# Kernel optimization log

Hardware: AMD Instinct MI355X
Metric: run time of the kernel (lower is better)

## Reference

```python
import jax, jax.numpy as jnp
import numpy as np

NHEAD = 16
EPS = 1e-6

def _phi_norm(x):
    # phi = silu, then L2 normalize over last dim (torch F.normalize: x / max(||x||, eps))
    x = jax.nn.silu(x)
    n = jnp.linalg.norm(x, axis=-1, keepdims=True)
    return x / jnp.maximum(n, EPS)

def setup_inputs() -> dict:
    key = jax.random.key(0)
    k1, k2, k3 = jax.random.split(key, 3)
    B, M, N, D = 4, 1024, 2048, 1024
    q = jax.random.normal(k1, (B, M, D), dtype=jnp.float32)
    kv = jax.random.normal(k2, (B, N, D), dtype=jnp.float32)
    kv_mask = jax.random.bernoulli(k3, 0.1, (B, N))  # True = masked out
    return {"q": q, "kv": kv, "kv_mask": kv_mask}

def reference(q, kv, kv_mask):
    B, M, D = q.shape
    N = kv.shape[1]
    dh = D // NHEAD
    # [B, H, M, dh] / [B, H, N, dh]
    qh = q.reshape(B, M, NHEAD, dh).transpose(0, 2, 1, 3)
    kh = kv.reshape(B, N, NHEAD, dh).transpose(0, 2, 1, 3)
    vh = kh  # values are raw kv heads (no phi/norm)
    qh_n = _phi_norm(qh)
    kh_n = _phi_norm(kh)
    scores = jnp.einsum('bhmd,bhnd->bhmn', qh_n, kh_n) / jnp.sqrt(jnp.asarray(dh, qh_n.dtype))
    scores = jnp.where(kv_mask[:, None, None, :], -jnp.inf, scores)
    attn = jax.nn.softmax(scores.astype(jnp.float32), axis=-1).astype(scores.dtype)
    out = jnp.einsum('bhmn,bhnd->bhmd', attn, vh)
    return out.transpose(0, 2, 1, 3).reshape(B, M, D)
```

## Files before the change

kernel.cpp:

```cpp
#include <hip/hip_runtime.h>
#include <hip/hip_bf16.h>
#include <cmath>
#include <stdint.h>

#define B_ 4
#define M_ 1024
#define N_ 2048
#define D_ 1024
#define H_ 16
#define DH_ 64
#define NT 64
#define NTH 16
#define PITCH 72

typedef __bf16 bf16_t;
typedef __attribute__((ext_vector_type(8))) __bf16 bf16x8;
typedef __attribute__((ext_vector_type(16))) float f32x16;

static __device__ __forceinline__ float silu_f(float x) {
  return x / (1.0f + __expf(-x));
}

#if __has_builtin(__builtin_amdgcn_exp2f)
#define EXP2F(x) __builtin_amdgcn_exp2f(x)
#else
#define EXP2F(x) __expf((x) * 0.69314718056f)
#endif

static __device__ __forceinline__ unsigned pk2(float a, float b) {
  union { __bf16 h[2]; unsigned u; } p;
  p.h[0] = (__bf16)a; p.h[1] = (__bf16)b;
  return p.u;
}

static __device__ __forceinline__ void pl32swap(unsigned &x, unsigned &y) {
  asm("s_nop 0\n\tv_permlane32_swap_b32 %0, %1" : "+v"(x), "+v"(y));
}

static __device__ __forceinline__ void gload16(const bf16_t* g, bf16_t* l) {
  typedef __attribute__((address_space(1))) const unsigned GU;
  typedef __attribute__((address_space(3))) unsigned LU;
  __builtin_amdgcn_global_load_lds((GU*)(const unsigned*)g, (LU*)(unsigned*)l,
                                   16, 0, 0);
}

__global__ __launch_bounds__(256) void prep_kernel(
    const float* __restrict__ kv, const int* __restrict__ kv_mask,
    bf16_t* __restrict__ kp, bf16_t* __restrict__ vt,
    unsigned long long* __restrict__ mb) {
  __shared__ __align__(16) bf16_t Lt[NT][PITCH];
  const int bx = blockIdx.x;
  const int hp = bx & 7;
  const int nt = (bx >> 3) & 31;
  const int b  = bx >> 8;
  const int n0 = nt * NT;
  const int tid = threadIdx.x;
  const float keep = kv_mask[b * N_ + n0 + (tid >> 2)] ? 0.f : 1.f;

  #pragma unroll
  for (int hi = 0; hi < 2; ++hi) {
    const int h = hp * 2 + hi;
    const size_t bh = (size_t)(b * H_ + h);
    {
      const int r = tid >> 2, c0 = (tid & 3) * 16;
      const float* src = kv + ((size_t)(b * N_ + n0 + r)) * D_ + h * DH_ + c0;
      union { float f[16]; float4 v4[4]; } raw;
      raw.v4[0] = *(const float4*)(src + 0);
      raw.v4[1] = *(const float4*)(src + 4);
      raw.v4[2] = *(const float4*)(src + 8);
      raw.v4[3] = *(const float4*)(src + 12);
      float sv[16];
      float ss = 0.f;
      #pragma unroll
      for (int i = 0; i < 16; ++i) { sv[i] = silu_f(raw.f[i]); ss += sv[i] * sv[i]; }
      ss += __shfl_xor(ss, 1); ss += __shfl_xor(ss, 2);
      const float inv = keep / fmaxf(sqrtf(ss), 1e-6f);
      union { bf16_t bs[16]; uint4 u[2]; } pk;
      #pragma unroll
      for (int i = 0; i < 16; ++i) pk.bs[i] = (bf16_t)(sv[i] * inv);
      uint4* kdst = (uint4*)(kp + (bh * N_ + n0 + r) * DH_ + c0);
      kdst[0] = pk.u[0]; kdst[1] = pk.u[1];
      union { bf16_t bs[16]; uint4 u[2]; } pv;
      #pragma unroll
      for (int i = 0; i < 16; ++i) pv.bs[i] = (bf16_t)(raw.f[i] * keep);
      uint4* ldst = (uint4*)&Lt[r][c0];
      ldst[0] = pv.u[0]; ldst[1] = pv.u[1];
    }
    __syncthreads();
    {
      const int d = tid >> 2, nc = (tid & 3) * 16;
      union { bf16_t bs[16]; uint4 u[2]; } pk;
      #pragma unroll
      for (int i = 0; i < 16; ++i) pk.bs[i] = Lt[nc + i][d];
      uint4* dst = (uint4*)(vt + (bh * DH_ + d) * N_ + n0 + nc);
      dst[0] = pk.u[0]; dst[1] = pk.u[1];
    }
    __syncthreads();
  }
  if (bx == 0 && tid < B_ * (N_ / 64)) {
    const int b2 = tid >> 5, tt = tid & 31;
    unsigned long long m = 0ull;
    for (int i = 0; i < 64; ++i)
      if (kv_mask[b2 * N_ + tt * 64 + i]) m |= (1ull << i);
    mb[tid] = m;
  }
}

__global__ __launch_bounds__(512, 4) void attn_kernel(
    const float* __restrict__ q, const bf16_t* __restrict__ kp,
    const bf16_t* __restrict__ vt, const unsigned long long* __restrict__ mb,
    float* __restrict__ out) {
  __shared__ __align__(1024) char smem[65536];

  const int tid  = threadIdx.x;
  const int w    = tid >> 6;
  const int wq   = w & 3;
  const int half = w >> 2;
  const int lane = tid & 63;
  const int l31  = lane & 31;
  const int hi   = lane >> 5;
  const int rho  = l31 & 7;

  const int wg = (blockIdx.x & 7) * 64 + (blockIdx.x >> 3);
  const int bh = wg >> 3;
  const int m0 = (wg & 7) * 128;
  const int b = bh >> 4, h = bh & 15;

  const bf16_t* kpb = kp + (size_t)bh * N_ * DH_ + (size_t)half * NTH * NT * DH_;
  const bf16_t* vtb = vt + (size_t)bh * DH_ * N_;

  const int srow  = lane >> 3;
  const int sslot = (lane & 7) ^ srow;
  const bf16_t* ks0 = kpb + (size_t)(wq * 16 + srow) * DH_ + sslot * 8;
  const bf16_t* ks1 = ks0 + 8 * DH_;
  const bf16_t* vs0 = vtb + (size_t)(wq * 16 + srow) * N_ + half * NTH * NT + sslot * 8;
  const bf16_t* vs1 = vs0 + 8 * N_;

  {
    bf16_t* Kd = (bf16_t*)(smem + (half * 2 + 0) * 8192) + wq * 16 * DH_;
    bf16_t* Vd = (bf16_t*)(smem + 32768 + (half * 2 + 0) * 8192) + wq * 16 * NT;
    gload16(ks0, Kd); gload16(ks1, Kd + 512);
    gload16(vs0, Vd); gload16(vs1, Vd + 512);
  }

  bf16x8 qb[4];
  {
    const float* qrow =
        q + ((size_t)(b * M_ + m0 + wq * 32 + l31)) * D_ + h * DH_ + hi * 8;
    float sv[32];
    float ss = 0.f;
    #pragma unroll
    for (int kk = 0; kk < 4; ++kk) {
      float4 a0 = *(const float4*)(qrow + kk * 16);
      float4 a1 = *(const float4*)(qrow + kk * 16 + 4);
      sv[kk * 8 + 0] = silu_f(a0.x); sv[kk * 8 + 1] = silu_f(a0.y);
      sv[kk * 8 + 2] = silu_f(a0.z); sv[kk * 8 + 3] = silu_f(a0.w);
      sv[kk * 8 + 4] = silu_f(a1.x); sv[kk * 8 + 5] = silu_f(a1.y);
      sv[kk * 8 + 6] = silu_f(a1.z); sv[kk * 8 + 7] = silu_f(a1.w);
      #pragma unroll
      for (int i = 0; i < 8; ++i) ss += sv[kk * 8 + i] * sv[kk * 8 + i];
    }
    ss += __shfl_xor(ss, 32);
    const float inv = 1.0f / fmaxf(sqrtf(ss), 1e-6f);
    #pragma unroll
    for (int kk = 0; kk < 4; ++kk) {
      union { unsigned u[4]; bf16x8 v; } pq;
      #pragma unroll
      for (int jj = 0; jj < 4; ++jj)
        pq.u[jj] = pk2(sv[kk * 8 + jj * 2] * inv, sv[kk * 8 + jj * 2 + 1] * inv);
      qb[kk] = pq.v;
    }
  }

  int foff[2][4];
  #pragma unroll
  for (int i = 0; i < 2; ++i)
    #pragma unroll
    for (int j = 0; j < 4; ++j)
      foff[i][j] = (i * 32 + l31) * 64 + ((((j << 1) + hi) ^ rho) << 3);

  f32x16 o0, o1;
  #pragma unroll
  for (int r = 0; r < 16; ++r) { o0[r] = 0.f; o1[r] = 0.f; }
  float lrun = 0.f;
  unsigned cl = 0, ch = 0;
  const unsigned long long* mbb = mb + b * (N_ / 64);
  const float C1 = 0.125f * 1.44269504f;

  for (int tt = 0; tt < NTH; ++tt) {
    __syncthreads();
    const int cur = tt & 1;
    if (tt + 1 < NTH) {
      const int nx = cur ^ 1;
      const size_t ko = (size_t)(tt + 1) * NT * DH_;
      const size_t vo = (size_t)(tt + 1) * NT;
      bf16_t* Kd = (bf16_t*)(smem + (half * 2 + nx) * 8192) + wq * 16 * DH_;
      bf16_t* Vd = (bf16_t*)(smem + 32768 + (half * 2 + nx) * 8192) + wq * 16 * NT;
      gload16(ks0 + ko, Kd); gload16(ks1 + ko, Kd + 512);
      gload16(vs0 + vo, Vd); gload16(vs1 + vo, Vd + 512);
    }
    const unsigned long long mk = mbb[half * NTH + tt];
    cl += (unsigned)__popcll(mk & 0x0F0F0F0F0F0F0F0FULL);
    ch += (unsigned)__popcll(mk & 0xF0F0F0F0F0F0F0F0ULL);

    const bf16_t* Kc = (const bf16_t*)(smem + (half * 2 + cur) * 8192);
    const bf16_t* Vc = (const bf16_t*)(smem + 32768 + (half * 2 + cur) * 8192);

    bf16x8 pa[4];
    #pragma unroll
    for (int nb = 0; nb < 2; ++nb) {
      f32x16 s;
      #pragma unroll
      for (int r = 0; r < 16; ++r) s[r] = 0.f;
      __builtin_amdgcn_s_setprio(1);
      #pragma unroll
      for (int kk = 0; kk < 4; ++kk) {
        bf16x8 ka = *(const bf16x8*)(Kc + foff[nb][kk]);
        s = __builtin_amdgcn_mfma_f32_32x32x16_bf16(ka, qb[kk], s, 0, 0, 0);
      }
      __builtin_amdgcn_s_setprio(0);

      float p[16];
      #pragma unroll
      for (int r = 0; r < 16; ++r) p[r] = EXP2F(s[r] * C1);
      lrun += (((p[0] + p[1]) + (p[2] + p[3])) + ((p[4] + p[5]) + (p[6] + p[7]))) +
              (((p[8] + p[9]) + (p[10] + p[11])) + ((p[12] + p[13]) + (p[14] + p[15])));

      unsigned pkw[4][2];
      #pragma unroll
      for (int qq = 0; qq < 4; ++qq) {
        pkw[qq][0] = pk2(p[qq * 4 + 0], p[qq * 4 + 1]);
        pkw[qq][1] = pk2(p[qq * 4 + 2], p[qq * 4 + 3]);
      }
      #pragma unroll
      for (int tp = 0; tp < 2; ++tp) {
        union { unsigned u[4]; bf16x8 v; } fr;
        #pragma unroll
        for (int ww = 0; ww < 2; ++ww) {
          const unsigned own = hi ? pkw[2 * tp + 1][ww] : pkw[2 * tp][ww];
          unsigned x = hi ? pkw[2 * tp][ww] : pkw[2 * tp + 1][ww];
          unsigned y = x;
          pl32swap(x, y);
          fr.u[ww]     = hi ? x : own;
          fr.u[2 + ww] = hi ? own : y;
        }
        pa[nb * 2 + tp] = fr.v;
      }
    }

    __builtin_amdgcn_s_setprio(1);
    #pragma unroll
    for (int ks = 0; ks < 4; ++ks) {
      bf16x8 vb0 = *(const bf16x8*)(Vc + foff[0][ks]);
      bf16x8 vb1 = *(const bf16x8*)(Vc + foff[1][ks]);
      o0 = __builtin_amdgcn_mfma_f32_32x32x16_bf16(pa[ks], vb0, o0, 0, 0, 0);
      o1 = __builtin_amdgcn_mfma_f32_32x32x16_bf16(pa[ks], vb1, o1, 0, 0, 0);
    }
    __builtin_amdgcn_s_setprio(0);
  }

  lrun -= (float)(hi ? ch : cl);
  __syncthreads();
  lrun += __shfl_xor(lrun, 32);
  float* Ob = (float*)smem;
  float* Lb = (float*)(smem + 32768);

  if (half == 0) {
    #pragma unroll
    for (int r = 0; r < 16; ++r) {
      const int mrow = (r & 3) + ((r >> 2) << 3) + (hi << 2);
      Ob[(wq * 32 + mrow) * 64 + l31]      = o0[r];
      Ob[(wq * 32 + mrow) * 64 + 32 + l31] = o1[r];
    }
    if (hi == 0) Lb[wq * 32 + l31] = lrun;
  }
  __syncthreads();
  if (half == 1) {
    const float ltot = lrun + Lb[wq * 32 + l31];
    #pragma unroll
    for (int r = 0; r < 16; ++r) {
      const int mrow = (r & 3) + ((r >> 2) << 3) + (hi << 2);
      const float lv = __shfl(ltot, mrow);
      const float iv = lv > 0.f ? 1.0f / lv : 0.f;
      const float oa = Ob[(wq * 32 + mrow) * 64 + l31];
      const float oc = Ob[(wq * 32 + mrow) * 64 + 32 + l31];
      const size_t base =
          ((size_t)(b * M_ + m0 + wq * 32 + mrow)) * D_ + h * DH_ + l31;
      out[base]      = (o0[r] + oa) * iv;
      out[base + 32] = (o1[r] + oc) * iv;
    }
  }
}

extern "C" void kernel_launch(void* const* d_in, const int* in_sizes, int n_in,
                              void* d_out, int out_size, void* d_ws, size_t ws_size,
                              hipStream_t stream) {
  const float* q  = (const float*)d_in[0];
  const float* kv = (const float*)d_in[1];
  const int* kv_mask = (const int*)d_in[2];
  float* out = (float*)d_out;

  bf16_t* kp = (bf16_t*)d_ws;
  bf16_t* vt = kp + (size_t)B_ * H_ * N_ * DH_;
  unsigned long long* mb =
      (unsigned long long*)((char*)d_ws + 2 * (size_t)B_ * H_ * N_ * DH_ * sizeof(bf16_t));

  prep_kernel<<<B_ * 32 * 8, 256, 0, stream>>>(kv, kv_mask, kp, vt, mb);
  attn_kernel<<<B_ * H_ * (M_ / 128), 512, 0, stream>>>(q, kp, vt, mb, out);
}
```

Baseline: 147.3 us.

## Replace exp2 with quadratic polynomial, permute K rows to drop permlane swaps

New measurement: 146.9 us. About the same (-0.3%).

```diff
diff --git a/kernel.cpp b/kernel.cpp
--- a/kernel.cpp
+++ b/kernel.cpp
@@ -16,25 +16,16 @@
 typedef __bf16 bf16_t;
 typedef __attribute__((ext_vector_type(8))) __bf16 bf16x8;
 typedef __attribute__((ext_vector_type(16))) float f32x16;
+typedef __attribute__((ext_vector_type(2))) float f32x2;
 
 static __device__ __forceinline__ float silu_f(float x) {
   return x / (1.0f + __expf(-x));
 }
-
-#if __has_builtin(__builtin_amdgcn_exp2f)
-#define EXP2F(x) __builtin_amdgcn_exp2f(x)
-#else
-#define EXP2F(x) __expf((x) * 0.69314718056f)
-#endif
 
 static __device__ __forceinline__ unsigned pk2(float a, float b) {
   union { __bf16 h[2]; unsigned u; } p;
   p.h[0] = (__bf16)a; p.h[1] = (__bf16)b;
   return p.u;
-}
-
-static __device__ __forceinline__ void pl32swap(unsigned &x, unsigned &y) {
-  asm("s_nop 0\n\tv_permlane32_swap_b32 %0, %1" : "+v"(x), "+v"(y));
 }
 
 static __device__ __forceinline__ void gload16(const bf16_t* g, bf16_t* l) {
@@ -42,6 +33,10 @@
   typedef __attribute__((address_space(3))) unsigned LU;
   __builtin_amdgcn_global_load_lds((GU*)(const unsigned*)g, (LU*)(unsigned*)l,
                                    16, 0, 0);
+}
+
+static __device__ __forceinline__ int sw23(int x) {
+  return (x & ~12) | ((x & 4) << 1) | ((x & 8) >> 1);
 }
 
 __global__ __launch_bounds__(256) void prep_kernel(
@@ -131,8 +126,8 @@
 
   const int srow  = lane >> 3;
   const int sslot = (lane & 7) ^ srow;
-  const bf16_t* ks0 = kpb + (size_t)(wq * 16 + srow) * DH_ + sslot * 8;
-  const bf16_t* ks1 = ks0 + 8 * DH_;
+  const bf16_t* ks0 = kpb + (size_t)sw23(wq * 16 + srow) * DH_ + sslot * 8;
+  const bf16_t* ks1 = kpb + (size_t)sw23(wq * 16 + 8 + srow) * DH_ + sslot * 8;
   const bf16_t* vs0 = vtb + (size_t)(wq * 16 + srow) * N_ + half * NTH * NT + sslot * 8;
   const bf16_t* vs1 = vs0 + 8 * N_;
 
@@ -161,7 +156,7 @@
       for (int i = 0; i < 8; ++i) ss += sv[kk * 8 + i] * sv[kk * 8 + i];
     }
     ss += __shfl_xor(ss, 32);
-    const float inv = 1.0f / fmaxf(sqrtf(ss), 1e-6f);
+    const float inv = 0.125f / fmaxf(sqrtf(ss), 1e-6f);
     #pragma unroll
     for (int kk = 0; kk < 4; ++kk) {
       union { unsigned u[4]; bf16x8 v; } pq;
@@ -179,13 +174,12 @@
     for (int j = 0; j < 4; ++j)
       foff[i][j] = (i * 32 + l31) * 64 + ((((j << 1) + hi) ^ rho) << 3);
 
-  f32x16 o0, o1;
+  f32x16 o0, o1, zvec;
   #pragma unroll
-  for (int r = 0; r < 16; ++r) { o0[r] = 0.f; o1[r] = 0.f; }
+  for (int r = 0; r < 16; ++r) { o0[r] = 0.f; o1[r] = 0.f; zvec[r] = 0.f; }
   float lrun = 0.f;
   unsigned cl = 0, ch = 0;
   const unsigned long long* mbb = mb + b * (N_ / 64);
-  const float C1 = 0.125f * 1.44269504f;
 
   for (int tt = 0; tt < NTH; ++tt) {
     __syncthreads();
@@ -200,8 +194,8 @@
       gload16(vs0 + vo, Vd); gload16(vs1 + vo, Vd + 512);
     }
     const unsigned long long mk = mbb[half * NTH + tt];
-    cl += (unsigned)__popcll(mk & 0x0F0F0F0F0F0F0F0FULL);
-    ch += (unsigned)__popcll(mk & 0xF0F0F0F0F0F0F0F0ULL);
+    cl += (unsigned)__popcll(mk & 0x00FF00FF00FF00FFULL);
+    ch += (unsigned)__popcll(mk & 0xFF00FF00FF00FF00ULL);
 
     const bf16_t* Kc = (const bf16_t*)(smem + (half * 2 + cur) * 8192);
     const bf16_t* Vc = (const bf16_t*)(smem + 32768 + (half * 2 + cur) * 8192);
@@ -209,43 +203,36 @@
     bf16x8 pa[4];
     #pragma unroll
     for (int nb = 0; nb < 2; ++nb) {
-      f32x16 s;
-      #pragma unroll
-      for (int r = 0; r < 16; ++r) s[r] = 0.f;
       __builtin_amdgcn_s_setprio(1);
-      #pragma unroll
-      for (int kk = 0; kk < 4; ++kk) {
+      f32x16 s = __builtin_amdgcn_mfma_f32_32x32x16_bf16(
+          *(const bf16x8*)(Kc + foff[nb][0]), qb[0], zvec, 0, 0, 0);
+      #pragma unroll
+      for (int kk = 1; kk < 4; ++kk) {
         bf16x8 ka = *(const bf16x8*)(Kc + foff[nb][kk]);
         s = __builtin_amdgcn_mfma_f32_32x32x16_bf16(ka, qb[kk], s, 0, 0, 0);
       }
       __builtin_amdgcn_s_setprio(0);
 
-      float p[16];
-      #pragma unroll
-      for (int r = 0; r < 16; ++r) p[r] = EXP2F(s[r] * C1);
-      lrun += (((p[0] + p[1]) + (p[2] + p[3])) + ((p[4] + p[5]) + (p[6] + p[7]))) +
-              (((p[8] + p[9]) + (p[10] + p[11])) + ((p[12] + p[13]) + (p[14] + p[15])));
-
-      unsigned pkw[4][2];
-      #pragma unroll
-      for (int qq = 0; qq < 4; ++qq) {
-        pkw[qq][0] = pk2(p[qq * 4 + 0], p[qq * 4 + 1]);
-        pkw[qq][1] = pk2(p[qq * 4 + 2], p[qq * 4 + 3]);
+      f32x2 p2[8];
+      #pragma unroll
+      for (int i = 0; i < 8; ++i) {
+        f32x2 x; x.x = s[2 * i]; x.y = s[2 * i + 1];
+        f32x2 u = x * 0.5f + 1.0f;
+        p2[i] = x * u + 1.0f;
       }
-      #pragma unroll
-      for (int tp = 0; tp < 2; ++tp) {
-        union { unsigned u[4]; bf16x8 v; } fr;
-        #pragma unroll
-        for (int ww = 0; ww < 2; ++ww) {
-          const unsigned own = hi ? pkw[2 * tp + 1][ww] : pkw[2 * tp][ww];
-          unsigned x = hi ? pkw[2 * tp][ww] : pkw[2 * tp + 1][ww];
-          unsigned y = x;
-          pl32swap(x, y);
-          fr.u[ww]     = hi ? x : own;
-          fr.u[2 + ww] = hi ? own : y;
-        }
-        pa[nb * 2 + tp] = fr.v;
+      f32x2 t0 = (p2[0] + p2[1]) + (p2[2] + p2[3]);
+      f32x2 t1 = (p2[4] + p2[5]) + (p2[6] + p2[7]);
+      f32x2 ts = t0 + t1;
+      lrun += ts.x + ts.y;
+
+      union { unsigned u[4]; bf16x8 v; } f0, f1;
+      #pragma unroll
+      for (int jj = 0; jj < 4; ++jj) {
+        f0.u[jj] = pk2(p2[jj].x, p2[jj].y);
+        f1.u[jj] = pk2(p2[4 + jj].x, p2[4 + jj].y);
       }
+      pa[nb * 2]     = f0.v;
+      pa[nb * 2 + 1] = f1.v;
     }
 
     __builtin_amdgcn_s_setprio(1);
@@ -253,41 +240,52 @@
     for (int ks = 0; ks < 4; ++ks) {
       bf16x8 vb0 = *(const bf16x8*)(Vc + foff[0][ks]);
       bf16x8 vb1 = *(const bf16x8*)(Vc + foff[1][ks]);
-      o0 = __builtin_amdgcn_mfma_f32_32x32x16_bf16(pa[ks], vb0, o0, 0, 0, 0);
-      o1 = __builtin_amdgcn_mfma_f32_32x32x16_bf16(pa[ks], vb1, o1, 0, 0, 0);
+      o0 = __builtin_amdgcn_mfma_f32_32x32x16_bf16(vb0, pa[ks], o0, 0, 0, 0);
+      o1 = __builtin_amdgcn_mfma_f32_32x32x16_bf16(vb1, pa[ks], o1, 0, 0, 0);
     }
     __builtin_amdgcn_s_setprio(0);
   }
 
   lrun -= (float)(hi ? ch : cl);
+  lrun += __shfl_xor(lrun, 32);
+
   __syncthreads();
-  lrun += __shfl_xor(lrun, 32);
   float* Ob = (float*)smem;
   float* Lb = (float*)(smem + 32768);
 
   if (half == 0) {
     #pragma unroll
     for (int r = 0; r < 16; ++r) {
-      const int mrow = (r & 3) + ((r >> 2) << 3) + (hi << 2);
-      Ob[(wq * 32 + mrow) * 64 + l31]      = o0[r];
-      Ob[(wq * 32 + mrow) * 64 + 32 + l31] = o1[r];
+      const int d = (r & 3) + ((r >> 2) << 3) + (hi << 2);
+      Ob[d * 128 + wq * 32 + l31]        = o0[r];
+      Ob[(d + 32) * 128 + wq * 32 + l31] = o1[r];
     }
     if (hi == 0) Lb[wq * 32 + l31] = lrun;
   }
   __syncthreads();
   if (half == 1) {
-    const float ltot = lrun + Lb[wq * 32 + l31];
     #pragma unroll
     for (int r = 0; r < 16; ++r) {
-      const int mrow = (r & 3) + ((r >> 2) << 3) + (hi << 2);
-      const float lv = __shfl(ltot, mrow);
-      const float iv = lv > 0.f ? 1.0f / lv : 0.f;
-      const float oa = Ob[(wq * 32 + mrow) * 64 + l31];
-      const float oc = Ob[(wq * 32 + mrow) * 64 + 32 + l31];
-      const size_t base =
-          ((size_t)(b * M_ + m0 + wq * 32 + mrow)) * D_ + h * DH_ + l31;
-      out[base]      = (o0[r] + oa) * iv;
-      out[base + 32] = (o1[r] + oc) * iv;
+      const int d = (r & 3) + ((r >> 2) << 3) + (hi << 2);
+      Ob[d * 128 + wq * 32 + l31]        += o0[r];
+      Ob[(d + 32) * 128 + wq * 32 + l31] += o1[r];
+    }
+    if (hi == 0) Lb[wq * 32 + l31] += lrun;
+  }
+  __syncthreads();
+  {
+    const int m = tid >> 2, dc = (tid & 3) * 16;
+    const float lv = Lb[m];
+    const float iv = lv > 0.f ? 1.0f / lv : 0.f;
+    float* orow = out + ((size_t)(b * M_ + m0 + m)) * D_ + h * DH_ + dc;
+    #pragma unroll
+    for (int i0 = 0; i0 < 16; i0 += 4) {
+      float4 v;
+      v.x = Ob[(dc + i0 + 0) * 128 + m] * iv;
+      v.y = Ob[(dc + i0 + 1) * 128 + m] * iv;
+      v.z = Ob[(dc + i0 + 2) * 128 + m] * iv;
+      v.w = Ob[(dc + i0 + 3) * 128 + m] * iv;
+      *(float4*)(orow + i0) = v;
     }
   }
 }
```
